# Performance work log

Hardware: AMD Instinct MI355X
Metric: run time of the kernel (lower is better)

Reference implementation:

```python
import jax, jax.numpy as jnp
import numpy as np

DIM = 1024
HEADS = 16
HEAD_DIM = DIM // HEADS  # 64


def get_rope_matrix(seq_len: int, dim: int) -> jnp.ndarray:
    # rope[s, d] = concat(cos(s * inv_freq), sin(s * inv_freq))  -> (seq_len, dim)
    half = dim // 2
    inv_freq = 1.0 / (10000.0 ** (jnp.arange(half, dtype=jnp.float32) / half))
    sinusoid = jnp.arange(seq_len, dtype=jnp.float32)[:, None] * inv_freq[None, :]
    return jnp.concatenate([jnp.cos(sinusoid), jnp.sin(sinusoid)], axis=-1)


def setup_inputs() -> dict:
    key = jax.random.key(0)
    ks = jax.random.split(key, 6)
    B, T, D = 2, 2048, DIM
    scale = 1.0 / np.sqrt(D)
    return {
        "x": jax.random.normal(ks[0], (B, T, D), dtype=jnp.float32),
        "Wq": jax.random.normal(ks[1], (D, D), dtype=jnp.float32) * scale,
        "Wk": jax.random.normal(ks[2], (D, D), dtype=jnp.float32) * scale,
        "Wv": jax.random.normal(ks[3], (D, D), dtype=jnp.float32) * scale,
        "Wo": jax.random.normal(ks[4], (D, D), dtype=jnp.float32) * scale,
        "bo": jax.random.normal(ks[5], (D,), dtype=jnp.float32) * 0.01,
    }


def reference(x, Wq, Wk, Wv, Wo, bo):
    B, T, D = x.shape
    H, hd = HEADS, HEAD_DIM

    # projections -> (B, H, T, hd)
    def split_heads(y):
        return y.reshape(B, T, H, hd).transpose(0, 2, 1, 3)

    q = split_heads(x @ Wq)
    k = split_heads(x @ Wk)
    v = split_heads(x @ Wv)

    rope = get_rope_matrix(T, hd)  # (T, hd)

    # apply_rope(v, rope): einsum('...nd,sd->...ns') contracts head_dim -> (B,H,T,T)
    v_r = jnp.einsum('bhnd,sd->bhns', v, rope)

    scores = jax.nn.softmax(jnp.einsum('bhnd,bhmd->bhnm', q, k) / jnp.sqrt(jnp.float32(hd)), axis=-1)
    out = jnp.einsum('bhnm,bhms->bhns', scores, v_r)  # (B,H,T,T)

    # apply_rope(out, rope.T): out2[...,n,s] = sum_t out[...,n,t] * rope[t,s] -> (B,H,T,hd)
    out = jnp.einsum('bhnt,ts->bhns', out, rope)

    out = out.transpose(0, 2, 1, 3).reshape(B, T, D)
    return out @ Wo + bo
```

## Files before the change

kernel.cpp:

```cpp
#include <hip/hip_runtime.h>
#include <math.h>

#define DIM 1024
#define NH 16
#define HD 64
#define TT 2048
#define NTOK 4096

typedef __bf16 bf8v __attribute__((ext_vector_type(8)));
typedef float f4v __attribute__((ext_vector_type(4)));
typedef unsigned short us8 __attribute__((ext_vector_type(8)));
typedef unsigned short us4 __attribute__((ext_vector_type(4)));

static __device__ __forceinline__ unsigned short f2bf(float f) {
    unsigned int u = __float_as_uint(f);
    u += 0x7FFFu + ((u >> 16) & 1u);
    return (unsigned short)(u >> 16);
}
static __device__ __forceinline__ bf8v ld8(const unsigned short* p) {
    return __builtin_bit_cast(bf8v, *(const us8*)p);
}

__global__ void k_prep(const float* __restrict__ x, unsigned short* __restrict__ xb,
                       const float* __restrict__ Wq, const float* __restrict__ Wk,
                       const float* __restrict__ Wv, unsigned short* __restrict__ wt,
                       float* __restrict__ rope) {
    int tid = threadIdx.x;
    int bb = blockIdx.x;
    if (bb < 4096) {
        int i = bb * 256 + tid;
        float4 v = ((const float4*)x)[i];
        us4 o;
        o[0] = f2bf(v.x); o[1] = f2bf(v.y); o[2] = f2bf(v.z); o[3] = f2bf(v.w);
        *(us4*)&xb[i * 4] = o;
    } else if (bb < 7168) {
        __shared__ float tile[32][33];
        bb -= 4096;
        int z = bb >> 10, rem = bb & 1023;
        int bx = rem & 31, by = rem >> 5;
        const float* W = (z == 0) ? Wq : ((z == 1) ? Wk : Wv);
        int tx = tid & 31, ty = tid >> 5;
        int c0 = bx * 32, k0 = by * 32;
#pragma unroll
        for (int j = 0; j < 4; j++)
            tile[ty + j * 8][tx] = W[(k0 + ty + j * 8) * DIM + c0 + tx];
        __syncthreads();
        unsigned short* out = wt + z * DIM * DIM;
#pragma unroll
        for (int j = 0; j < 4; j++)
            out[(c0 + ty + j * 8) * DIM + k0 + tx] = f2bf(tile[tx][ty + j * 8]);
    } else {
        int i = (bb - 7168) * 256 + tid;
        int s = i >> 6, d = i & 63;
        float inv = exp2f(-(float)(d & 31) * (13.287712379549449f / 32.0f));
        float a = (float)s * inv;
        rope[i] = (d < 32) ? cosf(a) : sinf(a);
    }
}

__global__ void k_R(const float* __restrict__ rope, float* __restrict__ R) {
    __shared__ float red[256];
    int d = blockIdx.x;
    int e = threadIdx.x & 63, sl = threadIdx.x >> 6;
    const float* rp = rope + sl * 512 * 64;
    float acc = 0.f;
    for (int s = 0; s < 512; s++)
        acc += rp[s * 64 + d] * rp[s * 64 + e];
    red[threadIdx.x] = acc;
    __syncthreads();
    if (sl == 0)
        R[d * 64 + e] = (red[e] + red[e + 64]) + (red[e + 128] + red[e + 192]);
}

__global__ void k_wo2(const float* __restrict__ Wo, const float* __restrict__ R,
                      unsigned short* __restrict__ wo2t) {
    __shared__ float Rt[64 * 64];
    int tid = threadIdx.x;
#pragma unroll
    for (int i = 0; i < 16; i++) {
        int idx = tid + i * 256;
        int e = idx >> 6, d = idx & 63;
        Rt[idx] = R[d * 64 + e];
    }
    __syncthreads();
    int j = blockIdx.x;
    float acc[4] = {0.f, 0.f, 0.f, 0.f};
    for (int e = 0; e < 64; e++) {
#pragma unroll
        for (int kk = 0; kk < 4; kk++) {
            int r = tid + kk * 256;
            int h = r >> 6, d = r & 63;
            acc[kk] += Rt[e * 64 + d] * Wo[(h * 64 + e) * DIM + j];
        }
    }
#pragma unroll
    for (int kk = 0; kk < 4; kk++)
        wo2t[j * DIM + tid + kk * 256] = f2bf(acc[kk]);
}

#define BK 32
#define LDA 40

__global__ __launch_bounds__(256, 3) void k_gemm_qkv(const unsigned short* __restrict__ A,
                                                     const unsigned short* __restrict__ Bt,
                                                     unsigned short* __restrict__ qk,
                                                     unsigned short* __restrict__ vt) {
    __shared__ unsigned short As[128 * LDA];
    __shared__ unsigned short Bs[128 * LDA];
    const int K = 1024;
    int tid = threadIdx.x;
    int lane = tid & 63, w = tid >> 6;
    int quad = lane >> 4, l16 = lane & 15;
    int m0 = blockIdx.y * 128, n0 = blockIdx.x * 128;
    int sr = tid >> 1, sc = (tid & 1) * 16;
    const unsigned short* Ag = A + (m0 + sr) * K + sc;
    const unsigned short* Bg = Bt + (n0 + sr) * K + sc;
    int wm = (w >> 1) * 64, wn = (w & 1) * 64;

    us8 a0 = *(const us8*)(Ag);
    us8 a1 = *(const us8*)(Ag + 8);
    us8 b0 = *(const us8*)(Bg);
    us8 b1 = *(const us8*)(Bg + 8);

    f4v acc[4][4] = {};
    for (int k0 = 0; k0 < K; k0 += BK) {
        __syncthreads();
        *(us8*)&As[sr * LDA + sc] = a0;
        *(us8*)&As[sr * LDA + sc + 8] = a1;
        *(us8*)&Bs[sr * LDA + sc] = b0;
        *(us8*)&Bs[sr * LDA + sc + 8] = b1;
        __syncthreads();
        if (k0 + BK < K) {
            a0 = *(const us8*)(Ag + k0 + BK);
            a1 = *(const us8*)(Ag + k0 + BK + 8);
            b0 = *(const us8*)(Bg + k0 + BK);
            b1 = *(const us8*)(Bg + k0 + BK + 8);
        }
        bf8v af[4], bf[4];
#pragma unroll
        for (int mt = 0; mt < 4; mt++)
            af[mt] = ld8(&As[(wm + mt * 16 + l16) * LDA + quad * 8]);
#pragma unroll
        for (int nt = 0; nt < 4; nt++)
            bf[nt] = ld8(&Bs[(wn + nt * 16 + l16) * LDA + quad * 8]);
#pragma unroll
        for (int mt = 0; mt < 4; mt++)
#pragma unroll
            for (int nt = 0; nt < 4; nt++)
                acc[mt][nt] = __builtin_amdgcn_mfma_f32_16x16x32_bf16(af[mt], bf[nt], acc[mt][nt], 0, 0, 0);
    }
#pragma unroll
    for (int mt = 0; mt < 4; mt++) {
#pragma unroll
        for (int nt = 0; nt < 4; nt++) {
            int gc = n0 + wn + nt * 16 + l16;
            int h = (gc >> 6) & 15;
            int d = gc & 63;
            if (gc < 2048) {
                float qs = (gc < 1024) ? 0.18033688011111793f : 1.0f;
                int mtx = gc >> 10;
                unsigned short* base = qk + mtx * (NTOK * DIM);
#pragma unroll
                for (int r = 0; r < 4; r++) {
                    int gm = m0 + wm + mt * 16 + quad * 4 + r;
                    int b = gm >> 11, t = gm & 2047;
                    base[((b * NH + h) * TT + t) * HD + d] = f2bf(acc[mt][nt][r] * qs);
                }
            } else {
                int gm0 = m0 + wm + mt * 16 + quad * 4;
                int b = gm0 >> 11, t = gm0 & 2047;
                us4 ov;
#pragma unroll
                for (int r = 0; r < 4; r++)
                    ov[r] = f2bf(acc[mt][nt][r]);
                *(us4*)&vt[(((b * NH + h) * HD) + d) * TT + t] = ov;
            }
        }
    }
}

__global__ __launch_bounds__(256, 3) void k_gemm_out(const unsigned short* __restrict__ A,
                                                     const unsigned short* __restrict__ Bt,
                                                     const float* __restrict__ bo,
                                                     float* __restrict__ out) {
    __shared__ unsigned short As[128 * LDA];
    __shared__ unsigned short Bs[128 * LDA];
    const int K = 1024;
    int tid = threadIdx.x;
    int lane = tid & 63, w = tid >> 6;
    int quad = lane >> 4, l16 = lane & 15;
    int m0 = blockIdx.y * 128, n0 = blockIdx.x * 128;
    int sr = tid >> 1, sc = (tid & 1) * 16;
    const unsigned short* Ag = A + (m0 + sr) * K + sc;
    const unsigned short* Bg = Bt + (n0 + sr) * K + sc;
    int wm = (w >> 1) * 64, wn = (w & 1) * 64;

    us8 a0 = *(const us8*)(Ag);
    us8 a1 = *(const us8*)(Ag + 8);
    us8 b0 = *(const us8*)(Bg);
    us8 b1 = *(const us8*)(Bg + 8);

    f4v acc[4][4] = {};
    for (int k0 = 0; k0 < K; k0 += BK) {
        __syncthreads();
        *(us8*)&As[sr * LDA + sc] = a0;
        *(us8*)&As[sr * LDA + sc + 8] = a1;
        *(us8*)&Bs[sr * LDA + sc] = b0;
        *(us8*)&Bs[sr * LDA + sc + 8] = b1;
        __syncthreads();
        if (k0 + BK < K) {
            a0 = *(const us8*)(Ag + k0 + BK);
            a1 = *(const us8*)(Ag + k0 + BK + 8);
            b0 = *(const us8*)(Bg + k0 + BK);
            b1 = *(const us8*)(Bg + k0 + BK + 8);
        }
        bf8v af[4], bf[4];
#pragma unroll
        for (int mt = 0; mt < 4; mt++)
            af[mt] = ld8(&As[(wm + mt * 16 + l16) * LDA + quad * 8]);
#pragma unroll
        for (int nt = 0; nt < 4; nt++)
            bf[nt] = ld8(&Bs[(wn + nt * 16 + l16) * LDA + quad * 8]);
#pragma unroll
        for (int mt = 0; mt < 4; mt++)
#pragma unroll
            for (int nt = 0; nt < 4; nt++)
                acc[mt][nt] = __builtin_amdgcn_mfma_f32_16x16x32_bf16(af[mt], bf[nt], acc[mt][nt], 0, 0, 0);
    }
#pragma unroll
    for (int mt = 0; mt < 4; mt++) {
#pragma unroll
        for (int nt = 0; nt < 4; nt++) {
            int gc = n0 + wn + nt * 16 + l16;
            float bias = bo[gc];
#pragma unroll
            for (int r = 0; r < 4; r++) {
                int gm = m0 + wm + mt * 16 + quad * 4 + r;
                out[gm * DIM + gc] = acc[mt][nt][r] + bias;
            }
        }
    }
}

#define LQ 72
__global__ __launch_bounds__(256, 4) void k_flash(const unsigned short* __restrict__ qk,
                                                  const unsigned short* __restrict__ vt,
                                                  unsigned short* __restrict__ attn) {
    __shared__ unsigned short Ks[64 * LQ];
    __shared__ unsigned short Vs[80 * LQ];
    __shared__ unsigned short Ps[128 * LQ];
    int tid = threadIdx.x;
    int lane = tid & 63, w = tid >> 6;
    int quad = lane >> 4, l16 = lane & 15;
    int bh = blockIdx.x & 31, qt = blockIdx.x >> 5;
    const unsigned short* Qg = qk + bh * (TT * HD);
    const unsigned short* Kg = qk + NTOK * DIM + bh * (TT * HD);
    const unsigned short* Vtg = vt + bh * (HD * TT);

    for (int idx = tid; idx < 16 * LQ; idx += 256)
        Vs[64 * LQ + idx] = (idx < LQ) ? (unsigned short)0x3F80 : (unsigned short)0;

    {
        int r = tid >> 1, c0 = (tid & 1) * 32;
        const us8* src = (const us8*)(Qg + (qt * 128 + r) * HD + c0);
#pragma unroll
        for (int i = 0; i < 4; i++)
            *(us8*)&Ps[r * LQ + c0 + i * 8] = src[i];
    }
    bf8v qf[2][2];
#pragma unroll
    for (int g = 0; g < 2; g++)
#pragma unroll
        for (int ks = 0; ks < 2; ks++)
            qf[g][ks] = ld8(&Ps[(w * 32 + g * 16 + l16) * LQ + ks * 32 + quad * 8]);

    int sr = tid >> 2, sc = (tid & 3) * 16;
    const unsigned short* Kgp = Kg + sr * HD + sc;
    const unsigned short* Vgp = Vtg + sr * TT + sc;
    us8 kr0 = *(const us8*)(Kgp);
    us8 kr1 = *(const us8*)(Kgp + 8);
    us8 vr0 = *(const us8*)(Vgp);
    us8 vr1 = *(const us8*)(Vgp + 8);

    f4v oacc[5][2] = {};

    for (int it = 0; it < 32; it++) {
        __syncthreads();
        *(us8*)&Ks[sr * LQ + sc] = kr0;
        *(us8*)&Ks[sr * LQ + sc + 8] = kr1;
        *(us8*)&Vs[sr * LQ + sc] = vr0;
        *(us8*)&Vs[sr * LQ + sc + 8] = vr1;
        __syncthreads();
        if (it < 31) {
            Kgp += 64 * HD;
            Vgp += 64;
            kr0 = *(const us8*)(Kgp);
            kr1 = *(const us8*)(Kgp + 8);
            vr0 = *(const us8*)(Vgp);
            vr1 = *(const us8*)(Vgp + 8);
        }

        f4v sacc[4][2] = {};
#pragma unroll
        for (int ks = 0; ks < 2; ks++) {
            bf8v kf[4];
#pragma unroll
            for (int mt = 0; mt < 4; mt++)
                kf[mt] = ld8(&Ks[(mt * 16 + l16) * LQ + ks * 32 + quad * 8]);
#pragma unroll
            for (int mt = 0; mt < 4; mt++)
#pragma unroll
                for (int g = 0; g < 2; g++)
                    sacc[mt][g] = __builtin_amdgcn_mfma_f32_16x16x32_bf16(kf[mt], qf[g][ks], sacc[mt][g], 0, 0, 0);
        }

#pragma unroll
        for (int g = 0; g < 2; g++) {
#pragma unroll
            for (int mt = 0; mt < 4; mt++) {
                float p0 = __builtin_amdgcn_exp2f(sacc[mt][g][0]);
                float p1 = __builtin_amdgcn_exp2f(sacc[mt][g][1]);
                float p2 = __builtin_amdgcn_exp2f(sacc[mt][g][2]);
                float p3 = __builtin_amdgcn_exp2f(sacc[mt][g][3]);
                unsigned int d0 = __builtin_amdgcn_perm(__float_as_uint(p1), __float_as_uint(p0), 0x07060302u);
                unsigned int d1 = __builtin_amdgcn_perm(__float_as_uint(p3), __float_as_uint(p2), 0x07060302u);
                uint2 pk; pk.x = d0; pk.y = d1;
                *(uint2*)&Ps[(w * 32 + g * 16 + l16) * LQ + mt * 16 + quad * 4] = pk;
            }
        }

#pragma unroll
        for (int ks = 0; ks < 2; ks++) {
            bf8v pf[2];
#pragma unroll
            for (int g = 0; g < 2; g++)
                pf[g] = ld8(&Ps[(w * 32 + g * 16 + l16) * LQ + ks * 32 + quad * 8]);
#pragma unroll
            for (int mtd = 0; mtd < 5; mtd++) {
                bf8v vf = ld8(&Vs[(mtd * 16 + l16) * LQ + ks * 32 + quad * 8]);
#pragma unroll
                for (int g = 0; g < 2; g++)
                    oacc[mtd][g] = __builtin_amdgcn_mfma_f32_16x16x32_bf16(vf, pf[g], oacc[mtd][g], 0, 0, 0);
            }
        }
    }

    int b = bh >> 4, h = bh & 15;
#pragma unroll
    for (int g = 0; g < 2; g++) {
        float ssum = __shfl(oacc[4][g][0], l16);
        float inv = 1.0f / ssum;
        int t = qt * 128 + w * 32 + g * 16 + l16;
        unsigned short* dst = attn + (b * TT + t) * DIM + h * HD;
#pragma unroll
        for (int mtd = 0; mtd < 4; mtd++) {
            us4 ov;
#pragma unroll
            for (int r = 0; r < 4; r++)
                ov[r] = f2bf(oacc[mtd][g][r] * inv);
            *(us4*)&dst[mtd * 16 + quad * 4] = ov;
        }
    }
}

extern "C" void kernel_launch(void* const* d_in, const int* in_sizes, int n_in,
                              void* d_out, int out_size, void* d_ws, size_t ws_size,
                              hipStream_t stream) {
    const float* x  = (const float*)d_in[0];
    const float* Wq = (const float*)d_in[1];
    const float* Wk = (const float*)d_in[2];
    const float* Wv = (const float*)d_in[3];
    const float* Wo = (const float*)d_in[4];
    const float* bo = (const float*)d_in[5];
    float* out = (float*)d_out;
    char* ws = (char*)d_ws;

    unsigned short* Xb    = (unsigned short*)(ws);
    unsigned short* Wqkvt = (unsigned short*)(ws + 8388608);
    unsigned short* QK    = (unsigned short*)(ws + 14680064);
    unsigned short* Vt    = (unsigned short*)(ws + 31457280);
    unsigned short* attn  = (unsigned short*)(ws + 39845888);
    unsigned short* Wo2t  = (unsigned short*)(ws + 48234496);
    float*          rope  = (float*)(ws + 50331648);
    float*          Rm    = (float*)(ws + 50855936);

    hipLaunchKernelGGL(k_prep,     dim3(7680),   dim3(256), 0, stream, x, Xb, Wq, Wk, Wv, Wqkvt, rope);
    hipLaunchKernelGGL(k_R,        dim3(64),     dim3(256), 0, stream, rope, Rm);
    hipLaunchKernelGGL(k_wo2,      dim3(1024),   dim3(256), 0, stream, Wo, Rm, Wo2t);
    hipLaunchKernelGGL(k_gemm_qkv, dim3(24, 32), dim3(256), 0, stream, Xb, Wqkvt, QK, Vt);
    hipLaunchKernelGGL(k_flash,    dim3(512),    dim3(256), 0, stream, QK, Vt, attn);
    hipLaunchKernelGGL(k_gemm_out, dim3(8, 32),  dim3(256), 0, stream, attn, Wo2t, bo, out);
}
```

Measured before the change: 225.2 us.

## Enlarge flash query tile to 256 rows and tile the Wo2 transform through LDS

The flash kernel now handles 256 query rows per block (64 per wave) instead of 128, so each loaded K/V tile feeds twice as many MFMAs and global K/V traffic is halved. The cost is more accumulators per thread, lower occupancy (launch bounds 2) and only 256 blocks on a large GPU. Separately, k_wo2 is retiled so each block stages a 64x64 Wo tile and R^T in padded shared memory, instead of doing strided uncached global reads of Wo per output column.

```diff
diff --git a/kernel.cpp b/kernel.cpp
--- a/kernel.cpp
+++ b/kernel.cpp
@@ -74,28 +74,27 @@
 
 __global__ void k_wo2(const float* __restrict__ Wo, const float* __restrict__ R,
                       unsigned short* __restrict__ wo2t) {
-    __shared__ float Rt[64 * 64];
-    int tid = threadIdx.x;
-#pragma unroll
-    for (int i = 0; i < 16; i++) {
-        int idx = tid + i * 256;
-        int e = idx >> 6, d = idx & 63;
-        Rt[idx] = R[d * 64 + e];
+    __shared__ float Ws[64 * 65];
+    __shared__ float Rt[64 * 65];
+    int tid = threadIdx.x;
+    int h = blockIdx.y, j0 = blockIdx.x * 64;
+    for (int idx = tid; idx < 4096; idx += 256) {
+        int e = idx >> 6, j = idx & 63;
+        Ws[e * 65 + j] = Wo[(h * 64 + e) * DIM + j0 + j];
+        Rt[e * 65 + j] = R[j * 64 + e];
     }
     __syncthreads();
-    int j = blockIdx.x;
-    float acc[4] = {0.f, 0.f, 0.f, 0.f};
+    int d = tid & 63, jb = (tid >> 6) * 16;
+    float acc[16] = {};
     for (int e = 0; e < 64; e++) {
-#pragma unroll
-        for (int kk = 0; kk < 4; kk++) {
-            int r = tid + kk * 256;
-            int h = r >> 6, d = r & 63;
-            acc[kk] += Rt[e * 64 + d] * Wo[(h * 64 + e) * DIM + j];
-        }
-    }
-#pragma unroll
-    for (int kk = 0; kk < 4; kk++)
-        wo2t[j * DIM + tid + kk * 256] = f2bf(acc[kk]);
+        float r = Rt[e * 65 + d];
+#pragma unroll
+        for (int jj = 0; jj < 16; jj++)
+            acc[jj] += r * Ws[e * 65 + jb + jj];
+    }
+#pragma unroll
+    for (int jj = 0; jj < 16; jj++)
+        wo2t[(j0 + jb + jj) * DIM + h * 64 + d] = f2bf(acc[jj]);
 }
 
 #define BK 32
@@ -243,12 +242,12 @@
 }
 
 #define LQ 72
-__global__ __launch_bounds__(256, 4) void k_flash(const unsigned short* __restrict__ qk,
+__global__ __launch_bounds__(256, 2) void k_flash(const unsigned short* __restrict__ qk,
                                                   const unsigned short* __restrict__ vt,
                                                   unsigned short* __restrict__ attn) {
     __shared__ unsigned short Ks[64 * LQ];
     __shared__ unsigned short Vs[80 * LQ];
-    __shared__ unsigned short Ps[128 * LQ];
+    __shared__ unsigned short Ps[256 * LQ];
     int tid = threadIdx.x;
     int lane = tid & 63, w = tid >> 6;
     int quad = lane >> 4, l16 = lane & 15;
@@ -261,18 +260,17 @@
         Vs[64 * LQ + idx] = (idx < LQ) ? (unsigned short)0x3F80 : (unsigned short)0;
 
     {
-        int r = tid >> 1, c0 = (tid & 1) * 32;
-        const us8* src = (const us8*)(Qg + (qt * 128 + r) * HD + c0);
-#pragma unroll
-        for (int i = 0; i < 4; i++)
-            *(us8*)&Ps[r * LQ + c0 + i * 8] = src[i];
-    }
-    bf8v qf[2][2];
-#pragma unroll
-    for (int g = 0; g < 2; g++)
+        const us8* src = (const us8*)(Qg + (qt * 256 + tid) * HD);
+#pragma unroll
+        for (int i = 0; i < 8; i++)
+            *(us8*)&Ps[tid * LQ + i * 8] = src[i];
+    }
+    bf8v qf[4][2];
+#pragma unroll
+    for (int g = 0; g < 4; g++)
 #pragma unroll
         for (int ks = 0; ks < 2; ks++)
-            qf[g][ks] = ld8(&Ps[(w * 32 + g * 16 + l16) * LQ + ks * 32 + quad * 8]);
+            qf[g][ks] = ld8(&Ps[(w * 64 + g * 16 + l16) * LQ + ks * 32 + quad * 8]);
 
     int sr = tid >> 2, sc = (tid & 3) * 16;
     const unsigned short* Kgp = Kg + sr * HD + sc;
@@ -282,7 +280,7 @@
     us8 vr0 = *(const us8*)(Vgp);
     us8 vr1 = *(const us8*)(Vgp + 8);
 
-    f4v oacc[5][2] = {};
+    f4v oacc[5][4] = {};
 
     for (int it = 0; it < 32; it++) {
         __syncthreads();
@@ -300,46 +298,45 @@
             vr1 = *(const us8*)(Vgp + 8);
         }
 
-        f4v sacc[4][2] = {};
-#pragma unroll
-        for (int ks = 0; ks < 2; ks++) {
-            bf8v kf[4];
+        bf8v kf[2][4];
+#pragma unroll
+        for (int ks = 0; ks < 2; ks++)
 #pragma unroll
             for (int mt = 0; mt < 4; mt++)
-                kf[mt] = ld8(&Ks[(mt * 16 + l16) * LQ + ks * 32 + quad * 8]);
-#pragma unroll
-            for (int mt = 0; mt < 4; mt++)
-#pragma unroll
-                for (int g = 0; g < 2; g++)
-                    sacc[mt][g] = __builtin_amdgcn_mfma_f32_16x16x32_bf16(kf[mt], qf[g][ks], sacc[mt][g], 0, 0, 0);
-        }
-
-#pragma unroll
-        for (int g = 0; g < 2; g++) {
+                kf[ks][mt] = ld8(&Ks[(mt * 16 + l16) * LQ + ks * 32 + quad * 8]);
+
+#pragma unroll
+        for (int g = 0; g < 4; g++) {
+            f4v sacc[4] = {};
+#pragma unroll
+            for (int ks = 0; ks < 2; ks++)
+#pragma unroll
+                for (int mt = 0; mt < 4; mt++)
+                    sacc[mt] = __builtin_amdgcn_mfma_f32_16x16x32_bf16(kf[ks][mt], qf[g][ks], sacc[mt], 0, 0, 0);
 #pragma unroll
             for (int mt = 0; mt < 4; mt++) {
-                float p0 = __builtin_amdgcn_exp2f(sacc[mt][g][0]);
-                float p1 = __builtin_amdgcn_exp2f(sacc[mt][g][1]);
-                float p2 = __builtin_amdgcn_exp2f(sacc[mt][g][2]);
-                float p3 = __builtin_amdgcn_exp2f(sacc[mt][g][3]);
+                float p0 = __builtin_amdgcn_exp2f(sacc[mt][0]);
+                float p1 = __builtin_amdgcn_exp2f(sacc[mt][1]);
+                float p2 = __builtin_amdgcn_exp2f(sacc[mt][2]);
+                float p3 = __builtin_amdgcn_exp2f(sacc[mt][3]);
                 unsigned int d0 = __builtin_amdgcn_perm(__float_as_uint(p1), __float_as_uint(p0), 0x07060302u);
                 unsigned int d1 = __builtin_amdgcn_perm(__float_as_uint(p3), __float_as_uint(p2), 0x07060302u);
                 uint2 pk; pk.x = d0; pk.y = d1;
-                *(uint2*)&Ps[(w * 32 + g * 16 + l16) * LQ + mt * 16 + quad * 4] = pk;
+                *(uint2*)&Ps[(w * 64 + g * 16 + l16) * LQ + mt * 16 + quad * 4] = pk;
             }
         }
 
 #pragma unroll
         for (int ks = 0; ks < 2; ks++) {
-            bf8v pf[2];
-#pragma unroll
-            for (int g = 0; g < 2; g++)
-                pf[g] = ld8(&Ps[(w * 32 + g * 16 + l16) * LQ + ks * 32 + quad * 8]);
+            bf8v pf[4];
+#pragma unroll
+            for (int g = 0; g < 4; g++)
+                pf[g] = ld8(&Ps[(w * 64 + g * 16 + l16) * LQ + ks * 32 + quad * 8]);
 #pragma unroll
             for (int mtd = 0; mtd < 5; mtd++) {
                 bf8v vf = ld8(&Vs[(mtd * 16 + l16) * LQ + ks * 32 + quad * 8]);
 #pragma unroll
-                for (int g = 0; g < 2; g++)
+                for (int g = 0; g < 4; g++)
                     oacc[mtd][g] = __builtin_amdgcn_mfma_f32_16x16x32_bf16(vf, pf[g], oacc[mtd][g], 0, 0, 0);
             }
         }
@@ -347,10 +344,10 @@
 
     int b = bh >> 4, h = bh & 15;
 #pragma unroll
-    for (int g = 0; g < 2; g++) {
+    for (int g = 0; g < 4; g++) {
         float ssum = __shfl(oacc[4][g][0], l16);
         float inv = 1.0f / ssum;
-        int t = qt * 128 + w * 32 + g * 16 + l16;
+        int t = qt * 256 + w * 64 + g * 16 + l16;
         unsigned short* dst = attn + (b * TT + t) * DIM + h * HD;
 #pragma unroll
         for (int mtd = 0; mtd < 4; mtd++) {
@@ -386,8 +383,8 @@
 
     hipLaunchKernelGGL(k_prep,     dim3(7680),   dim3(256), 0, stream, x, Xb, Wq, Wk, Wv, Wqkvt, rope);
     hipLaunchKernelGGL(k_R,        dim3(64),     dim3(256), 0, stream, rope, Rm);
-    hipLaunchKernelGGL(k_wo2,      dim3(1024),   dim3(256), 0, stream, Wo, Rm, Wo2t);
+    hipLaunchKernelGGL(k_wo2,      dim3(16, 16), dim3(256), 0, stream, Wo, Rm, Wo2t);
     hipLaunchKernelGGL(k_gemm_qkv, dim3(24, 32), dim3(256), 0, stream, Xb, Wqkvt, QK, Vt);
-    hipLaunchKernelGGL(k_flash,    dim3(512),    dim3(256), 0, stream, QK, Vt, attn);
+    hipLaunchKernelGGL(k_flash,    dim3(256),    dim3(256), 0, stream, QK, Vt, attn);
     hipLaunchKernelGGL(k_gemm_out, dim3(8, 32),  dim3(256), 0, stream, attn, Wo2t, bo, out);
 }
```

New measurement: 226.7 us. About the same (+0.7%).
